# Performance work log

Hardware: AMD Instinct MI355X
Metric: run time of the kernel (lower is better)

Reference implementation:

```python
import jax, jax.numpy as jnp
import numpy as np

EMBED = 256; HEADS = 8; LEVELS = 1; POINTS = 4; QUEUE = 2
HB = 200; WB = 200; NQ = HB * WB; BS = 1


def bilinear_sample(img, grid, h, w):
    # img: (BH, D, h*w) flattened feature map; grid: (BH, N, 2) in [-1, 1]
    # torch.grid_sample(align_corners=False, padding_mode='zeros') semantics
    gx, gy = grid[..., 0], grid[..., 1]
    x = (gx + 1.0) * (w * 0.5) - 0.5
    y = (gy + 1.0) * (h * 0.5) - 0.5
    x0 = jnp.floor(x); y0 = jnp.floor(y)
    lx = x - x0; ly = y - y0
    x0i = x0.astype(jnp.int32); y0i = y0.astype(jnp.int32)

    def corner(xi, yi, wgt):
        valid = ((xi >= 0) & (xi < w) & (yi >= 0) & (yi < h)).astype(img.dtype)
        idx = jnp.clip(yi, 0, h - 1) * w + jnp.clip(xi, 0, w - 1)  # (BH, N)
        vals = jax.vmap(lambda im, ix: im[:, ix])(img, idx)  # (BH, D, N)
        return vals * (wgt * valid)[:, None, :]

    return (corner(x0i, y0i, (1 - lx) * (1 - ly))
            + corner(x0i + 1, y0i, lx * (1 - ly))
            + corner(x0i, y0i + 1, (1 - lx) * ly)
            + corner(x0i + 1, y0i + 1, lx * ly))


def ms_deform_attn(value, shapes, loc, aw):
    # value: (B, Nv, H, D); loc: (B, nq, H, L, P, 2); aw: (B, nq, H, L, P)
    B, Nv, H, D = value.shape
    nq = loc.shape[1]; P = loc.shape[4]
    grids = 2.0 * loc - 1.0
    start = 0
    per_level = []
    for l in range(shapes.shape[0]):
        h, w = int(shapes[l, 0]), int(shapes[l, 1])
        vl = value[:, start:start + h * w].reshape(B, h, w, H, D)
        vl = vl.transpose(0, 3, 4, 1, 2).reshape(B * H, D, h * w)
        g = grids[:, :, :, l].transpose(0, 2, 1, 3, 4).reshape(B * H, nq * P, 2)
        samp = bilinear_sample(vl, g, h, w).reshape(B, H, D, nq, P)
        per_level.append(samp)
        start += h * w
    sampled = jnp.stack(per_level, axis=4)  # (B, H, D, nq, L, P)
    w_ = aw.transpose(0, 2, 1, 3, 4)[:, :, None]  # (B, H, 1, nq, L, P)
    out = (sampled * w_).sum(axis=(-1, -2))  # (B, H, D, nq)
    return out.reshape(B, H * D, nq).transpose(0, 2, 1)  # (B, nq, E)


def setup_inputs():
    key = jax.random.key(0)
    ks = jax.random.split(key, 10)
    s = 0.02
    n_off = QUEUE * HEADS * LEVELS * POINTS * 2
    n_aw = QUEUE * HEADS * LEVELS * POINTS
    return {
        "query": jax.random.normal(ks[0], (BS, NQ, EMBED), jnp.float32),
        "query_pos": jax.random.normal(ks[1], (BS, NQ, EMBED), jnp.float32),
        "value": jax.random.normal(ks[2], (BS * QUEUE, NQ, EMBED), jnp.float32),
        "reference_points": jax.random.uniform(ks[3], (BS * QUEUE, NQ, LEVELS, 2), jnp.float32),
        "spatial_shapes": jnp.array([[HB, WB]], dtype=jnp.int32),
        "W_off": jax.random.normal(ks[4], (EMBED * QUEUE, n_off), jnp.float32) * s,
        "b_off": jnp.zeros((n_off,), jnp.float32),
        "W_attn": jax.random.normal(ks[5], (EMBED * QUEUE, n_aw), jnp.float32) * s,
        "b_attn": jnp.zeros((n_aw,), jnp.float32),
        "W_val": jax.random.normal(ks[6], (EMBED, EMBED), jnp.float32) * s,
        "b_val": jnp.zeros((EMBED,), jnp.float32),
        "W_out": jax.random.normal(ks[7], (EMBED, EMBED), jnp.float32) * s,
        "b_out": jnp.zeros((EMBED,), jnp.float32),
    }


def reference(query, query_pos, value, reference_points, spatial_shapes,
              W_off, b_off, W_attn, b_attn, W_val, b_val, W_out, b_out):
    shapes = np.asarray(spatial_shapes)  # static level shapes
    bs, nq, E = query.shape
    identity = query
    q = query + query_pos
    # temporal query: concat current-frame value with query
    q2 = jnp.concatenate([value[:bs], q], axis=-1)  # (bs, nq, 2E)
    v = value @ W_val + b_val  # (bs*2, nv, E)
    nv = v.shape[1]
    v = v.reshape(bs * QUEUE, nv, HEADS, E // HEADS)
    off = (q2 @ W_off + b_off).reshape(bs, nq, HEADS, QUEUE, LEVELS, POINTS, 2)
    aw = (q2 @ W_attn + b_attn).reshape(bs, nq, HEADS, QUEUE, LEVELS * POINTS)
    aw = jax.nn.softmax(aw, axis=-1).reshape(bs, nq, HEADS, QUEUE, LEVELS, POINTS)
    aw = aw.transpose(0, 3, 1, 2, 4, 5).reshape(bs * QUEUE, nq, HEADS, LEVELS, POINTS)
    off = off.transpose(0, 3, 1, 2, 4, 5, 6).reshape(bs * QUEUE, nq, HEADS, LEVELS, POINTS, 2)
    # normalized sampling locations: (bs*2, nq, H, L, P, 2)
    normalizer = jnp.stack([spatial_shapes[..., 1], spatial_shapes[..., 0]], -1).astype(jnp.float32)
    loc = reference_points[:, :, None, :, None, :] + off / normalizer[None, None, None, :, None, :]
    out = ms_deform_attn(v, shapes, loc, aw)  # (bs*2, nq, E)
    # average over the BEV queue (current + history)
    out = out.transpose(1, 2, 0).reshape(nq, E, bs, QUEUE).mean(-1).transpose(2, 0, 1)
    out = out @ W_out + b_out
    return out + identity
```

## Files before the change

kernel.cpp:

```cpp
#include <hip/hip_runtime.h>
#include <math.h>

#define NQ    40000
#define EMB   256
#define NHEAD 8
#define HDIM  32
#define HB    200
#define WB    200
#define NCOL  192
#define HPIX  2560000

typedef __attribute__((ext_vector_type(8))) __bf16 bf16x8;
typedef __attribute__((ext_vector_type(4))) float f32x4;

static __device__ __forceinline__ unsigned short f2bf(float f) {
  unsigned u = __float_as_uint(f);
  u = u + 0x7fffu + ((u >> 16) & 1u);
  return (unsigned short)(u >> 16);
}
static __device__ __forceinline__ float bf2f(unsigned short s) {
  return __uint_as_float(((unsigned)s) << 16);
}
static __device__ __forceinline__ void acc8(float* a, uint4 u, float w) {
  a[0] += w * __uint_as_float(u.x << 16);
  a[1] += w * __uint_as_float(u.x & 0xffff0000u);
  a[2] += w * __uint_as_float(u.y << 16);
  a[3] += w * __uint_as_float(u.y & 0xffff0000u);
  a[4] += w * __uint_as_float(u.z << 16);
  a[5] += w * __uint_as_float(u.z & 0xffff0000u);
  a[6] += w * __uint_as_float(u.w << 16);
  a[7] += w * __uint_as_float(u.w & 0xffff0000u);
}

__global__ __launch_bounds__(256) void conv_w(
    const float* __restrict__ W_off, const float* __restrict__ b_off,
    const float* __restrict__ W_attn, const float* __restrict__ b_attn,
    const float* __restrict__ W_val, const float* __restrict__ W_out,
    unsigned short* __restrict__ Wc1t, unsigned short* __restrict__ Wvt,
    unsigned short* __restrict__ Wot, float* __restrict__ bc1)
{
  int idx = blockIdx.x * 256 + threadIdx.x;
  if (idx < 98304) {
    int n = idx >> 9, k = idx & 511;
    float v = (n < 128) ? W_off[(size_t)k * 128 + n] : W_attn[(size_t)k * 64 + (n - 128)];
    Wc1t[idx] = f2bf(v);
  } else if (idx < 163840) {
    int j = idx - 98304;
    int n = j >> 8, k = j & 255;
    Wvt[j] = f2bf(W_val[(size_t)k * 256 + n]);
  } else if (idx < 229376) {
    int j = idx - 163840;
    int n = j >> 8, k = j & 255;
    Wot[j] = f2bf(W_out[(size_t)k * 256 + n]);
  } else if (idx < 229568) {
    int n = idx - 229376;
    bc1[n] = (n < 128) ? b_off[n] : b_attn[n - 128];
  }
}

template<int K, int N, int AMODE, int OMODE, bool RESID>
__global__ __launch_bounds__(256, 4) void rb_gemm(
    const void* __restrict__ Aptr, const void* __restrict__ Aq2a,
    const void* __restrict__ Aq2b, const unsigned short* __restrict__ Bt,
    const float* __restrict__ bias, const float* __restrict__ resid,
    void* __restrict__ outp)
{
  constexpr int NFR = N / 64;
  constexpr int NP  = N + 8;
  constexpr int ATB = (AMODE != 0) ? 32 * K * 2 : 0;
  constexpr int TRB = (OMODE != 0) ? 32 * NP * 2 : 0;
  constexpr int MXB = (ATB > TRB) ? ATB : TRB;
  constexpr int LDSB = (MXB > 64) ? MXB : 64;
  __shared__ __align__(16) char lds[LDSB];
  unsigned short* trn = (unsigned short*)lds;

  const int t = threadIdx.x;
  const int m0 = blockIdx.x * 32;
  const int wid = t >> 6, lane = t & 63;
  const int wn = wid * (N / 4);
  const int lr = lane & 15, quad = lane >> 4;

  auto cvt_store = [&](int r, int c, float4 f0, float4 f1) {
    union { unsigned short us[8]; uint4 v; } u;
    u.us[0] = f2bf(f0.x); u.us[1] = f2bf(f0.y);
    u.us[2] = f2bf(f0.z); u.us[3] = f2bf(f0.w);
    u.us[4] = f2bf(f1.x); u.us[5] = f2bf(f1.y);
    u.us[6] = f2bf(f1.z); u.us[7] = f2bf(f1.w);
    *(uint4*)(lds + (size_t)r * (K * 2) + ((c ^ (r & 7)) * 16)) = u.v;
  };

  if constexpr (AMODE == 1) {
    const int c = t & 31, r0 = t >> 5;
    float4 f[4][2];
    #pragma unroll
    for (int l = 0; l < 4; l++) {
      const float* s = (const float*)Aptr + (size_t)(m0 + r0 + 8 * l) * K + c * 8;
      f[l][0] = *(const float4*)s; f[l][1] = *(const float4*)(s + 4);
    }
    #pragma unroll
    for (int l = 0; l < 4; l++)
      cvt_store(r0 + 8 * l, c, f[l][0], f[l][1]);
    __syncthreads();
  } else if constexpr (AMODE == 2) {
    const int c = t & 63, r0 = t >> 6;
    if (c < 32) {
      float4 f[8][2];
      #pragma unroll
      for (int l = 0; l < 8; l++) {
        const float* s = (const float*)Aptr + (size_t)(m0 + r0 + 4 * l) * 256 + c * 8;
        f[l][0] = *(const float4*)s; f[l][1] = *(const float4*)(s + 4);
      }
      #pragma unroll
      for (int l = 0; l < 8; l++)
        cvt_store(r0 + 4 * l, c, f[l][0], f[l][1]);
    } else {
      #pragma unroll
      for (int h = 0; h < 2; h++) {
        float4 fq[4][2], fp[4][2];
        #pragma unroll
        for (int l = 0; l < 4; l++) {
          int r = r0 + 4 * (h * 4 + l);
          const float* sq = (const float*)Aq2a + (size_t)(m0 + r) * 256 + (c - 32) * 8;
          const float* sp = (const float*)Aq2b + (size_t)(m0 + r) * 256 + (c - 32) * 8;
          fq[l][0] = *(const float4*)sq; fq[l][1] = *(const float4*)(sq + 4);
          fp[l][0] = *(const float4*)sp; fp[l][1] = *(const float4*)(sp + 4);
        }
        #pragma unroll
        for (int l = 0; l < 4; l++) {
          int r = r0 + 4 * (h * 4 + l);
          float4 f0 = make_float4(fq[l][0].x + fp[l][0].x, fq[l][0].y + fp[l][0].y,
                                  fq[l][0].z + fp[l][0].z, fq[l][0].w + fp[l][0].w);
          float4 f1 = make_float4(fq[l][1].x + fp[l][1].x, fq[l][1].y + fp[l][1].y,
                                  fq[l][1].z + fp[l][1].z, fq[l][1].w + fp[l][1].w);
          cvt_store(r, c, f0, f1);
        }
      }
    }
    __syncthreads();
  }

  f32x4 acc[2][NFR];
  #pragma unroll
  for (int i = 0; i < 2; i++)
    #pragma unroll
    for (int n = 0; n < NFR; n++) acc[i][n] = (f32x4){0.f, 0.f, 0.f, 0.f};

  auto loadB = [&](bf16x8* dst, int k0) {
    #pragma unroll
    for (int n = 0; n < NFR; n++)
      dst[n] = *(const bf16x8*)(Bt + (size_t)(wn + n * 16 + lr) * K + k0 + quad * 8);
  };
  auto loadA = [&](bf16x8* dst, int k0) {
    if constexpr (AMODE == 0) {
      const unsigned short* A = (const unsigned short*)Aptr;
      #pragma unroll
      for (int i = 0; i < 2; i++)
        dst[i] = *(const bf16x8*)(A + (size_t)(m0 + lr + i * 16) * K + k0 + quad * 8);
    } else {
      const int cb = (k0 >> 3) + quad;
      const int sw = (cb ^ (lr & 7)) * 16;
      #pragma unroll
      for (int i = 0; i < 2; i++)
        dst[i] = *(const bf16x8*)(lds + (size_t)(lr + i * 16) * (K * 2) + sw);
    }
  };

  constexpr int NK = K / 32;
  bf16x8 bcur[NFR], af[2];
  loadB(bcur, 0);
  loadA(af, 0);
  #pragma unroll
  for (int ks = 0; ks < NK; ks++) {
    bf16x8 bnxt[NFR], anxt[2];
    if (ks + 1 < NK) {
      loadB(bnxt, (ks + 1) * 32);
      loadA(anxt, (ks + 1) * 32);
    }
    #pragma unroll
    for (int i = 0; i < 2; i++)
      #pragma unroll
      for (int n = 0; n < NFR; n++)
        acc[i][n] = __builtin_amdgcn_mfma_f32_16x16x32_bf16(af[i], bcur[n], acc[i][n], 0, 0, 0);
    if (ks + 1 < NK) {
      #pragma unroll
      for (int n = 0; n < NFR; n++) bcur[n] = bnxt[n];
      af[0] = anxt[0]; af[1] = anxt[1];
    }
  }

  if constexpr (OMODE == 0) {
    #pragma unroll
    for (int i = 0; i < 2; i++) {
      int rowb = m0 + i * 16 + quad * 4;
      #pragma unroll
      for (int n = 0; n < NFR; n++) {
        int col = wn + n * 16 + lr;
        float bsv = bias[col];
        #pragma unroll
        for (int r = 0; r < 4; r++) {
          int rr = rowb + r;
          float v = acc[i][n][r] + bsv;
          if (RESID) v += resid[(size_t)rr * N + col];
          ((float*)outp)[(size_t)rr * N + col] = v;
        }
      }
    }
  } else {
    if constexpr (AMODE != 0) __syncthreads();
    #pragma unroll
    for (int i = 0; i < 2; i++) {
      #pragma unroll
      for (int n = 0; n < NFR; n++) {
        int col = wn + n * 16 + lr;
        float bsv = bias[col];
        #pragma unroll
        for (int r = 0; r < 4; r++) {
          int rl = i * 16 + quad * 4 + r;
          trn[rl * NP + col] = f2bf(acc[i][n][r] + bsv);
        }
      }
    }
    __syncthreads();
    constexpr int NCH = (32 * N) / 2048;
    #pragma unroll
    for (int l = 0; l < NCH; l++) {
      int c = t + l * 256;
      int row = c / (N / 8);
      int coloff = (c % (N / 8)) * 8;
      uint4 d = *(const uint4*)(trn + row * NP + coloff);
      unsigned short* op = (unsigned short*)outp;
      if constexpr (OMODE == 2)
        op += (size_t)(coloff >> 5) * HPIX + (size_t)(m0 + row) * 32 + (coloff & 31);
      else
        op += (size_t)(m0 + row) * N + coloff;
      *(uint4*)op = d;
    }
  }
}

__global__ __launch_bounds__(256) void k3_sample(
    const unsigned short* __restrict__ raw1, const float* __restrict__ refp,
    const unsigned short* __restrict__ vh, unsigned short* __restrict__ msd)
{
  __shared__ int4   sidx[8][64];
  __shared__ float4 swgt[8][64];
  const int t = threadIdx.x;
  const int q0 = blockIdx.x * 8;

  #pragma unroll
  for (int ee = 0; ee < 2; ee++) {
    const int e = t + ee * 256;
    const int qi = e >> 6, r6 = e & 63;
    const int b = r6 >> 5, h = (r6 >> 2) & 7, p = r6 & 3;
    const int q = q0 + qi;
    const unsigned short* r = raw1 + (size_t)q * NCOL;
    float ox = bf2f(r[h * 16 + b * 8 + p * 2 + 0]);
    float oy = bf2f(r[h * 16 + b * 8 + p * 2 + 1]);
    float l0 = bf2f(r[128 + h * 8 + b * 4 + 0]);
    float l1 = bf2f(r[128 + h * 8 + b * 4 + 1]);
    float l2 = bf2f(r[128 + h * 8 + b * 4 + 2]);
    float l3 = bf2f(r[128 + h * 8 + b * 4 + 3]);
    float mx = fmaxf(fmaxf(l0, l1), fmaxf(l2, l3));
    float e0 = expf(l0 - mx), e1 = expf(l1 - mx);
    float e2 = expf(l2 - mx), e3 = expf(l3 - mx);
    float ssum = e0 + e1 + e2 + e3;
    float ep = (p == 0) ? e0 : (p == 1) ? e1 : (p == 2) ? e2 : e3;
    float aw = ep / ssum * 0.5f;
    float rx = refp[((size_t)b * NQ + q) * 2 + 0];
    float ry = refp[((size_t)b * NQ + q) * 2 + 1];
    float px = rx * (float)WB + ox - 0.5f;
    float py = ry * (float)HB + oy - 0.5f;
    float x0f = floorf(px), y0f = floorf(py);
    float lx = px - x0f, ly = py - y0f;
    int x0 = (int)x0f, y0 = (int)y0f, x1 = x0 + 1, y1 = y0 + 1;
    int x0c = min(max(x0, 0), WB - 1), x1c = min(max(x1, 0), WB - 1);
    int y0c = min(max(y0, 0), HB - 1), y1c = min(max(y1, 0), HB - 1);
    float vx0 = ((unsigned)x0 < (unsigned)WB) ? 1.f : 0.f;
    float vx1 = ((unsigned)x1 < (unsigned)WB) ? 1.f : 0.f;
    float vy0 = ((unsigned)y0 < (unsigned)HB) ? 1.f : 0.f;
    float vy1 = ((unsigned)y1 < (unsigned)HB) ? 1.f : 0.f;
    const int pb = b * NQ;
    int4 ix;
    ix.x = pb + y0c * WB + x0c;
    ix.y = pb + y0c * WB + x1c;
    ix.z = pb + y1c * WB + x0c;
    ix.w = pb + y1c * WB + x1c;
    float4 wv;
    wv.x = aw * (1.f - lx) * (1.f - ly) * vx0 * vy0;
    wv.y = aw * lx * (1.f - ly) * vx1 * vy0;
    wv.z = aw * (1.f - lx) * ly * vx0 * vy1;
    wv.w = aw * lx * ly * vx1 * vy1;
    sidx[qi][r6] = ix;
    swgt[qi][r6] = wv;
  }
  __syncthreads();

  const int qi = t >> 5, h = (t >> 2) & 7, c = t & 3;
  const unsigned short* vb = vh + (size_t)h * HPIX + c * 8;
  float a[8];
  #pragma unroll
  for (int j = 0; j < 8; j++) a[j] = 0.f;
  #pragma unroll
  for (int b = 0; b < 2; b++) {
    #pragma unroll
    for (int p = 0; p < 4; p++) {
      int ent = b * 32 + h * 4 + p;
      int4 pix = sidx[qi][ent];
      float4 wv = swgt[qi][ent];
      uint4 v00 = *(const uint4*)(vb + (size_t)pix.x * 32);
      uint4 v10 = *(const uint4*)(vb + (size_t)pix.y * 32);
      uint4 v01 = *(const uint4*)(vb + (size_t)pix.z * 32);
      uint4 v11 = *(const uint4*)(vb + (size_t)pix.w * 32);
      acc8(a, v00, wv.x);
      acc8(a, v10, wv.y);
      acc8(a, v01, wv.z);
      acc8(a, v11, wv.w);
    }
  }
  union { unsigned short us[8]; uint4 v; } o;
  #pragma unroll
  for (int j = 0; j < 8; j++) o.us[j] = f2bf(a[j]);
  *(uint4*)(msd + (size_t)(q0 + qi) * EMB + h * HDIM + c * 8) = o.v;
}

extern "C" void kernel_launch(void* const* d_in, const int* in_sizes, int n_in,
                              void* d_out, int out_size, void* d_ws, size_t ws_size,
                              hipStream_t stream) {
  const float* query     = (const float*)d_in[0];
  const float* query_pos = (const float*)d_in[1];
  const float* value     = (const float*)d_in[2];
  const float* refp      = (const float*)d_in[3];
  const float* W_off  = (const float*)d_in[5];
  const float* b_off  = (const float*)d_in[6];
  const float* W_attn = (const float*)d_in[7];
  const float* b_attn = (const float*)d_in[8];
  const float* W_val  = (const float*)d_in[9];
  const float* b_val  = (const float*)d_in[10];
  const float* W_out  = (const float*)d_in[11];
  const float* b_out  = (const float*)d_in[12];
  float* out = (float*)d_out;

  char* ws = (char*)d_ws;
  unsigned short* raw1 = (unsigned short*)(ws);
  unsigned short* vout = (unsigned short*)(ws + 15360000);
  unsigned short* msdb = (unsigned short*)(ws + 56320000);
  unsigned short* Wc1t = (unsigned short*)(ws + 76800000);
  unsigned short* Wvt  = (unsigned short*)(ws + 76996608);
  unsigned short* Wot  = (unsigned short*)(ws + 77127680);
  float*          bc1  = (float*)(ws + 77258752);

  hipLaunchKernelGGL(conv_w, dim3(897), dim3(256), 0, stream,
                     W_off, b_off, W_attn, b_attn, W_val, W_out, Wc1t, Wvt, Wot, bc1);

  hipLaunchKernelGGL((rb_gemm<512, 192, 2, 1, false>),
                     dim3(1250), dim3(256), 0, stream,
                     (const void*)value, (const void*)query, (const void*)query_pos,
                     Wc1t, bc1, (const float*)nullptr, (void*)raw1);
  hipLaunchKernelGGL((rb_gemm<256, 256, 1, 2, false>),
                     dim3(2500), dim3(256), 0, stream,
                     (const void*)value, (const void*)nullptr, (const void*)nullptr,
                     Wvt, b_val, (const float*)nullptr, (void*)vout);
  hipLaunchKernelGGL(k3_sample, dim3(NQ / 8), dim3(256), 0, stream,
                     raw1, refp, vout, msdb);
  hipLaunchKernelGGL((rb_gemm<256, 256, 0, 0, true>),
                     dim3(1250), dim3(256), 0, stream,
                     (const void*)msdb, (const void*)nullptr, (const void*)nullptr,
                     Wot, b_out, query, (void*)out);
}
```

Measured before the change: 373.0 us.

## Make sampling blocks head-major and store sampled output in head-planar layout

The sampling kernel now gives each block a single head and 64 queries, where before each block covered 8 queries across all heads. Every block therefore gathers from only one head's value plane, which should improve cache locality for the scattered bilinear reads. The intermediate output is written in a head-planar layout ([head][query][32]), and the output GEMM gets a new A-load mode that reads that layout directly. The cost is 64-byte strided A loads in the final GEMM in place of contiguous rows.

After: 355.0 us. 4.8% less time.

```diff
diff --git a/kernel.cpp b/kernel.cpp
--- a/kernel.cpp
+++ b/kernel.cpp
@@ -21,15 +21,15 @@
 static __device__ __forceinline__ float bf2f(unsigned short s) {
   return __uint_as_float(((unsigned)s) << 16);
 }
-static __device__ __forceinline__ void acc8(float* a, uint4 u, float w) {
-  a[0] += w * __uint_as_float(u.x << 16);
-  a[1] += w * __uint_as_float(u.x & 0xffff0000u);
-  a[2] += w * __uint_as_float(u.y << 16);
-  a[3] += w * __uint_as_float(u.y & 0xffff0000u);
-  a[4] += w * __uint_as_float(u.z << 16);
-  a[5] += w * __uint_as_float(u.z & 0xffff0000u);
-  a[6] += w * __uint_as_float(u.w << 16);
-  a[7] += w * __uint_as_float(u.w & 0xffff0000u);
+static __device__ __forceinline__ void accp(float4& lo4, float4& hi4, uint4 u, float w) {
+  lo4.x += w * __uint_as_float(u.x << 16);
+  lo4.y += w * __uint_as_float(u.x & 0xffff0000u);
+  lo4.z += w * __uint_as_float(u.y << 16);
+  lo4.w += w * __uint_as_float(u.y & 0xffff0000u);
+  hi4.x += w * __uint_as_float(u.z << 16);
+  hi4.y += w * __uint_as_float(u.z & 0xffff0000u);
+  hi4.z += w * __uint_as_float(u.w << 16);
+  hi4.w += w * __uint_as_float(u.w & 0xffff0000u);
 }
 
 __global__ __launch_bounds__(256) void conv_w(
@@ -67,7 +67,7 @@
 {
   constexpr int NFR = N / 64;
   constexpr int NP  = N + 8;
-  constexpr int ATB = (AMODE != 0) ? 32 * K * 2 : 0;
+  constexpr int ATB = (AMODE == 1 || AMODE == 2) ? 32 * K * 2 : 0;
   constexpr int TRB = (OMODE != 0) ? 32 * NP * 2 : 0;
   constexpr int MXB = (ATB > TRB) ? ATB : TRB;
   constexpr int LDSB = (MXB > 64) ? MXB : 64;
@@ -115,11 +115,11 @@
         cvt_store(r0 + 4 * l, c, f[l][0], f[l][1]);
     } else {
       #pragma unroll
-      for (int h = 0; h < 2; h++) {
+      for (int hh = 0; hh < 2; hh++) {
         float4 fq[4][2], fp[4][2];
         #pragma unroll
         for (int l = 0; l < 4; l++) {
-          int r = r0 + 4 * (h * 4 + l);
+          int r = r0 + 4 * (hh * 4 + l);
           const float* sq = (const float*)Aq2a + (size_t)(m0 + r) * 256 + (c - 32) * 8;
           const float* sp = (const float*)Aq2b + (size_t)(m0 + r) * 256 + (c - 32) * 8;
           fq[l][0] = *(const float4*)sq; fq[l][1] = *(const float4*)(sq + 4);
@@ -127,7 +127,7 @@
         }
         #pragma unroll
         for (int l = 0; l < 4; l++) {
-          int r = r0 + 4 * (h * 4 + l);
+          int r = r0 + 4 * (hh * 4 + l);
           float4 f0 = make_float4(fq[l][0].x + fp[l][0].x, fq[l][0].y + fp[l][0].y,
                                   fq[l][0].z + fp[l][0].z, fq[l][0].w + fp[l][0].w);
           float4 f1 = make_float4(fq[l][1].x + fp[l][1].x, fq[l][1].y + fp[l][1].y,
@@ -156,6 +156,13 @@
       #pragma unroll
       for (int i = 0; i < 2; i++)
         dst[i] = *(const bf16x8*)(A + (size_t)(m0 + lr + i * 16) * K + k0 + quad * 8);
+    } else if constexpr (AMODE == 4) {
+      const unsigned short* A = (const unsigned short*)Aptr;
+      const int h = k0 >> 5;
+      #pragma unroll
+      for (int i = 0; i < 2; i++)
+        dst[i] = *(const bf16x8*)(A + (size_t)h * NQ * 32
+                                    + (size_t)(m0 + lr + i * 16) * 32 + quad * 8);
     } else {
       const int cb = (k0 >> 3) + quad;
       const int sw = (cb ^ (lr & 7)) * 16;
@@ -171,10 +178,10 @@
   loadA(af, 0);
   #pragma unroll
   for (int ks = 0; ks < NK; ks++) {
-    bf16x8 bnxt[NFR], anxt[2];
+    bf16x8 bn[NFR], an[2];
     if (ks + 1 < NK) {
-      loadB(bnxt, (ks + 1) * 32);
-      loadA(anxt, (ks + 1) * 32);
+      loadB(bn, (ks + 1) * 32);
+      loadA(an, (ks + 1) * 32);
     }
     #pragma unroll
     for (int i = 0; i < 2; i++)
@@ -183,8 +190,8 @@
         acc[i][n] = __builtin_amdgcn_mfma_f32_16x16x32_bf16(af[i], bcur[n], acc[i][n], 0, 0, 0);
     if (ks + 1 < NK) {
       #pragma unroll
-      for (int n = 0; n < NFR; n++) bcur[n] = bnxt[n];
-      af[0] = anxt[0]; af[1] = anxt[1];
+      for (int n = 0; n < NFR; n++) bcur[n] = bn[n];
+      af[0] = an[0]; af[1] = an[1];
     }
   }
 
@@ -206,7 +213,7 @@
       }
     }
   } else {
-    if constexpr (AMODE != 0) __syncthreads();
+    __syncthreads();
     #pragma unroll
     for (int i = 0; i < 2; i++) {
       #pragma unroll
@@ -242,16 +249,16 @@
     const unsigned short* __restrict__ raw1, const float* __restrict__ refp,
     const unsigned short* __restrict__ vh, unsigned short* __restrict__ msd)
 {
-  __shared__ int4   sidx[8][64];
-  __shared__ float4 swgt[8][64];
+  __shared__ int4   sidx[512];
+  __shared__ float4 swgt[512];
   const int t = threadIdx.x;
-  const int q0 = blockIdx.x * 8;
+  const int h  = blockIdx.x & 7;
+  const int q0 = (blockIdx.x >> 3) * 64;
 
   #pragma unroll
   for (int ee = 0; ee < 2; ee++) {
     const int e = t + ee * 256;
-    const int qi = e >> 6, r6 = e & 63;
-    const int b = r6 >> 5, h = (r6 >> 2) & 7, p = r6 & 3;
+    const int qi = e >> 3, b = (e >> 2) & 1, p = e & 3;
     const int q = q0 + qi;
     const unsigned short* r = raw1 + (size_t)q * NCOL;
     float ox = bf2f(r[h * 16 + b * 8 + p * 2 + 0]);
@@ -290,37 +297,33 @@
     wv.y = aw * lx * (1.f - ly) * vx1 * vy0;
     wv.z = aw * (1.f - lx) * ly * vx0 * vy1;
     wv.w = aw * lx * ly * vx1 * vy1;
-    sidx[qi][r6] = ix;
-    swgt[qi][r6] = wv;
+    sidx[e] = ix;
+    swgt[e] = wv;
   }
   __syncthreads();
 
-  const int qi = t >> 5, h = (t >> 2) & 7, c = t & 3;
+  const int qi = t >> 2, c = t & 3;
   const unsigned short* vb = vh + (size_t)h * HPIX + c * 8;
-  float a[8];
-  #pragma unroll
-  for (int j = 0; j < 8; j++) a[j] = 0.f;
+  float4 lo = {0.f, 0.f, 0.f, 0.f}, hi = lo;
   #pragma unroll
   for (int b = 0; b < 2; b++) {
     #pragma unroll
     for (int p = 0; p < 4; p++) {
-      int ent = b * 32 + h * 4 + p;
-      int4 pix = sidx[qi][ent];
-      float4 wv = swgt[qi][ent];
-      uint4 v00 = *(const uint4*)(vb + (size_t)pix.x * 32);
-      uint4 v10 = *(const uint4*)(vb + (size_t)pix.y * 32);
-      uint4 v01 = *(const uint4*)(vb + (size_t)pix.z * 32);
-      uint4 v11 = *(const uint4*)(vb + (size_t)pix.w * 32);
-      acc8(a, v00, wv.x);
-      acc8(a, v10, wv.y);
-      acc8(a, v01, wv.z);
-      acc8(a, v11, wv.w);
+      int ent = qi * 8 + b * 4 + p;
+      int4 pix = sidx[ent];
+      float4 wv = swgt[ent];
+      accp(lo, hi, *(const uint4*)(vb + (size_t)pix.x * 32), wv.x);
+      accp(lo, hi, *(const uint4*)(vb + (size_t)pix.y * 32), wv.y);
+      accp(lo, hi, *(const uint4*)(vb + (size_t)pix.z * 32), wv.z);
+      accp(lo, hi, *(const uint4*)(vb + (size_t)pix.w * 32), wv.w);
     }
   }
   union { unsigned short us[8]; uint4 v; } o;
-  #pragma unroll
-  for (int j = 0; j < 8; j++) o.us[j] = f2bf(a[j]);
-  *(uint4*)(msd + (size_t)(q0 + qi) * EMB + h * HDIM + c * 8) = o.v;
+  o.us[0] = f2bf(lo.x); o.us[1] = f2bf(lo.y);
+  o.us[2] = f2bf(lo.z); o.us[3] = f2bf(lo.w);
+  o.us[4] = f2bf(hi.x); o.us[5] = f2bf(hi.y);
+  o.us[6] = f2bf(hi.z); o.us[7] = f2bf(hi.w);
+  *(uint4*)(msd + (size_t)h * NQ * 32 + (size_t)(q0 + qi) * 32 + c * 8) = o.v;
 }
 
 extern "C" void kernel_launch(void* const* d_in, const int* in_sizes, int n_in,
@@ -360,9 +363,9 @@
                      dim3(2500), dim3(256), 0, stream,
                      (const void*)value, (const void*)nullptr, (const void*)nullptr,
                      Wvt, b_val, (const float*)nullptr, (void*)vout);
-  hipLaunchKernelGGL(k3_sample, dim3(NQ / 8), dim3(256), 0, stream,
+  hipLaunchKernelGGL(k3_sample, dim3(5000), dim3(256), 0, stream,
                      raw1, refp, vout, msdb);
-  hipLaunchKernelGGL((rb_gemm<256, 256, 0, 0, true>),
+  hipLaunchKernelGGL((rb_gemm<256, 256, 4, 0, true>),
                      dim3(1250), dim3(256), 0, stream,
                      (const void*)msdb, (const void*)nullptr, (const void*)nullptr,
                      Wot, b_out, query, (void*)out);
```
